# Performance work log

Hardware: AMD Instinct MI355X
Metric: run time of the kernel (lower is better)

Reference implementation:

```python
import jax, jax.numpy as jnp
import numpy as np

TEMPERATURE = 0.07
EPS = 1e-8  # torch CosineSimilarity eps


def setup_inputs() -> dict:
    key = jax.random.key(0)
    k1, k2, k3 = jax.random.split(key, 3)
    N, D = 8192, 512
    features = jax.random.normal(k1, (N, D), dtype=jnp.float32)
    positive_mask = jax.random.randint(k2, (N, N), 0, 2, dtype=jnp.int32)
    negative_mask = jax.random.randint(k3, (N, N), 0, 2, dtype=jnp.int32)
    return {"features": features, "positive_mask": positive_mask, "negative_mask": negative_mask}


def reference(features, positive_mask, negative_mask):
    N = positive_mask.shape[0]
    self_contrast = 1.0 - jnp.eye(N, dtype=features.dtype)  # zero diagonal
    pos = positive_mask.astype(features.dtype) * self_contrast  # [N, N]
    neg = negative_mask.astype(features.dtype) * self_contrast  # [N, N]

    # cosine similarity via normalized matmul (same math as broadcasted CosineSimilarity)
    norm = jnp.maximum(jnp.linalg.norm(features, axis=1, keepdims=True), EPS)
    fn = features / norm  # [N, D]
    sim = jnp.matmul(fn, fn.T) / TEMPERATURE  # [N, N]

    logits_max = jax.lax.stop_gradient(jnp.max(sim, axis=1, keepdims=True))
    e = jnp.exp(sim - logits_max)  # [N, N]

    positives = e * pos
    log_neg_sum = jnp.log(jnp.sum(e * neg, axis=1, keepdims=True))  # [N, 1]
    log_prob = positives - log_neg_sum  # [N, N] (faithful to source: exp-masked, not log)

    cardinal = jnp.sum(pos, axis=1)
    cardinal = jnp.where(cardinal == 0, 1.0, cardinal)
    log_prob_sum = jnp.sum(log_prob * pos, axis=1)
    loss = -log_prob_sum / cardinal
    return jnp.mean(loss)
```

## Files before the change

kernel.cpp:

```cpp
#include <hip/hip_runtime.h>
#include <hip/hip_bf16.h>
#include <math.h>

#define NN 8192
#define DD 512
#define INV_T 14.285714285714286f

typedef __attribute__((ext_vector_type(8))) short s16x8;
typedef __attribute__((ext_vector_type(4))) float f32x4;
typedef __attribute__((ext_vector_type(4))) int   i32x4;

__device__ __forceinline__ unsigned short f32_to_bf16(float f) {
  unsigned int u = __float_as_uint(f);
  u += 0x7FFFu + ((u >> 16) & 1u);
  return (unsigned short)(u >> 16);
}

__device__ __forceinline__ void async16(const void* g, void* l) {
  __builtin_amdgcn_global_load_lds((__attribute__((address_space(1))) void*)(void*)g,
                                   (__attribute__((address_space(3))) void*)l,
                                   16, 0, 0);
}

__global__ __launch_bounds__(256) void normalize_kernel(const float* __restrict__ f,
                                                        unsigned short* __restrict__ fnb) {
  const int wave = threadIdx.x >> 6;
  const int lane = threadIdx.x & 63;
  const int row  = blockIdx.x * 4 + wave;
  const float* src = f + (size_t)row * DD + lane * 8;
  float4 v0 = *(const float4*)src;
  float4 v1 = *(const float4*)(src + 4);
  float ss = v0.x*v0.x + v0.y*v0.y + v0.z*v0.z + v0.w*v0.w
           + v1.x*v1.x + v1.y*v1.y + v1.z*v1.z + v1.w*v1.w;
  #pragma unroll
  for (int o = 32; o; o >>= 1) ss += __shfl_xor(ss, o);
  const float r = 1.0f / fmaxf(sqrtf(ss), 1e-8f);
  ushort4 a, b;
  a.x = f32_to_bf16(v0.x * r); a.y = f32_to_bf16(v0.y * r);
  a.z = f32_to_bf16(v0.z * r); a.w = f32_to_bf16(v0.w * r);
  b.x = f32_to_bf16(v1.x * r); b.y = f32_to_bf16(v1.y * r);
  b.z = f32_to_bf16(v1.z * r); b.w = f32_to_bf16(v1.w * r);
  unsigned short* dst = fnb + (size_t)row * DD + lane * 8;
  *(ushort4*)dst = a;
  *(ushort4*)(dst + 4) = b;
}

__global__ __launch_bounds__(256, 3) void fused_kernel(const unsigned short* __restrict__ fnb,
                                                       const int* __restrict__ posm,
                                                       const int* __restrict__ negm,
                                                       float* __restrict__ Spos,
                                                       float* __restrict__ Sneg,
                                                       float* __restrict__ Pcnt) {
  const int bid = blockIdx.x;
  int bi = (int)(64.5 - sqrt(64.5 * 64.5 - 2.0 * (double)bid));
  while (64 * bi - bi * (bi - 1) / 2 > bid) --bi;
  while (64 * (bi + 1) - (bi + 1) * bi / 2 <= bid) ++bi;
  const int bj = bi + (bid - (64 * bi - bi * (bi - 1) / 2));
  const int I = bi * 128;
  const int J = bj * 128;
  const bool offdiag = (bi != bj);

  const int tid  = threadIdx.x;
  const int wave = tid >> 6;
  const int lane = tid & 63;
  const int wm = wave >> 1;
  const int wn = wave & 1;
  const int q   = lane >> 4;
  const int c16 = lane & 15;

  __shared__ alignas(16) unsigned short lA[128 * 32];
  __shared__ alignas(16) unsigned short lB[128 * 32];
  __shared__ float sacc[2][128][3];
  for (int t = tid; t < 2 * 128 * 3; t += 256) ((float*)sacc)[t] = 0.f;

  f32x4 acc[4][4];
  const f32x4 z4 = {0.f, 0.f, 0.f, 0.f};
  #pragma unroll
  for (int mt = 0; mt < 4; ++mt)
    #pragma unroll
    for (int nt = 0; nt < 4; ++nt) acc[mt][nt] = z4;

  for (int kk = 0; kk < DD / 32; ++kk) {
    const int k0 = kk * 32;
    #pragma unroll
    for (int c = 0; c < 2; ++c) {
      const int fidx = tid + c * 256;
      const int L    = fidx >> 2;
      const int p    = fidx & 3;
      const int csrc = (p ^ ((L >> 1) & 3)) & 3;
      async16(fnb + (size_t)(I + L) * DD + k0 + csrc * 8, (char*)lA + fidx * 16);
      const int gB = 4 * (L & 31) + (L >> 5);
      async16(fnb + (size_t)(J + gB) * DD + k0 + csrc * 8, (char*)lB + fidx * 16);
    }
    __syncthreads();

    s16x8 aF[4], bF[4];
    #pragma unroll
    for (int t = 0; t < 4; ++t) {
      const int arow = wm * 64 + t * 16 + c16;
      const int apos = (q ^ ((arow >> 1) & 3)) & 3;
      aF[t] = *(const s16x8*)((const char*)lA + arow * 64 + apos * 16);
      const int Lb = (wn * 16 + c16) | (t << 5);
      const int bpos = (q ^ ((Lb >> 1) & 3)) & 3;
      bF[t] = *(const s16x8*)((const char*)lB + Lb * 64 + bpos * 16);
    }
    #pragma unroll
    for (int mt = 0; mt < 4; ++mt)
      #pragma unroll
      for (int nt = 0; nt < 4; ++nt)
        acc[mt][nt] = __builtin_amdgcn_mfma_f32_16x16x32_bf16(aF[mt], bF[nt], acc[mt][nt], 0, 0, 0);
    __syncthreads();
  }

  #pragma unroll
  for (int mt = 0; mt < 4; ++mt)
    #pragma unroll
    for (int nt = 0; nt < 4; ++nt)
      #pragma unroll
      for (int r = 0; r < 4; ++r)
        acc[mt][nt][r] = __expf(acc[mt][nt][r] * INV_T - INV_T);

  const bool hasdiag = (bi == bj) && (wm == wn);
  const int cb = wn * 64 + 4 * c16;

  #pragma unroll
  for (int mt = 0; mt < 4; ++mt) {
    const int rl = wm * 64 + mt * 16 + q * 4;
    i32x4 pv[4], nv[4];
    #pragma unroll
    for (int r = 0; r < 4; ++r) {
      const size_t off = (size_t)(I + rl + r) * NN + J + cb;
      pv[r] = __builtin_nontemporal_load((const i32x4*)(posm + off));
      nv[r] = __builtin_nontemporal_load((const i32x4*)(negm + off));
    }
    #pragma unroll
    for (int r = 0; r < 4; ++r) {
      float dsp = 0.f, dsn = 0.f, dpc = 0.f;
      #pragma unroll
      for (int nt = 0; nt < 4; ++nt) {
        float pf = (float)pv[r][nt];
        float nf = (float)nv[r][nt];
        if (hasdiag && (rl + r == cb + nt)) { pf = 0.f; nf = 0.f; }
        const float e = acc[mt][nt][r];
        dsp = fmaf(e, pf, dsp);
        dsn = fmaf(e, nf, dsn);
        dpc += pf;
      }
      #pragma unroll
      for (int o = 1; o <= 8; o <<= 1) {
        dsp += __shfl_xor(dsp, o);
        dsn += __shfl_xor(dsn, o);
        dpc += __shfl_xor(dpc, o);
      }
      if (c16 == 0) {
        atomicAdd(&sacc[0][rl + r][0], dsp);
        atomicAdd(&sacc[0][rl + r][1], dsn);
        atomicAdd(&sacc[0][rl + r][2], dpc);
      }
    }
  }

  if (offdiag) {
    #pragma unroll
    for (int nt = 0; nt < 4; ++nt) {
      const int trl = cb + nt;
      i32x4 pv[4], nv[4];
      #pragma unroll
      for (int mt = 0; mt < 4; ++mt) {
        const size_t off = (size_t)(J + trl) * NN + I + wm * 64 + mt * 16 + q * 4;
        pv[mt] = __builtin_nontemporal_load((const i32x4*)(posm + off));
        nv[mt] = __builtin_nontemporal_load((const i32x4*)(negm + off));
      }
      float ts = 0.f, tn = 0.f, tp = 0.f;
      #pragma unroll
      for (int mt = 0; mt < 4; ++mt) {
        #pragma unroll
        for (int r = 0; r < 4; ++r) {
          const float e = acc[mt][nt][r];
          ts = fmaf(e, (float)pv[mt][r], ts);
          tn = fmaf(e, (float)nv[mt][r], tn);
          tp += (float)pv[mt][r];
        }
      }
      ts += __shfl_xor(ts, 16); ts += __shfl_xor(ts, 32);
      tn += __shfl_xor(tn, 16); tn += __shfl_xor(tn, 32);
      tp += __shfl_xor(tp, 16); tp += __shfl_xor(tp, 32);
      if (q == 0) {
        atomicAdd(&sacc[1][trl][0], ts);
        atomicAdd(&sacc[1][trl][1], tn);
        atomicAdd(&sacc[1][trl][2], tp);
      }
    }
  }

  __syncthreads();

  const int r = tid & 127;
  if (tid < 128) {
    atomicAdd(&Spos[I + r], sacc[0][r][0]);
    atomicAdd(&Sneg[I + r], sacc[0][r][1]);
    atomicAdd(&Pcnt[I + r], sacc[0][r][2]);
  } else if (offdiag) {
    atomicAdd(&Spos[J + r], sacc[1][r][0]);
    atomicAdd(&Sneg[J + r], sacc[1][r][1]);
    atomicAdd(&Pcnt[J + r], sacc[1][r][2]);
  }
}

__global__ __launch_bounds__(256) void finalize_kernel(const float* __restrict__ Spos,
                                                       const float* __restrict__ Sneg,
                                                       const float* __restrict__ Pcnt,
                                                       float* __restrict__ out) {
  float local = 0.f;
  for (int i = threadIdx.x; i < NN; i += 256) {
    const float sp = Spos[i], sn = Sneg[i], pc = Pcnt[i];
    const float card = (pc == 0.f) ? 1.f : pc;
    local += (logf(sn) * pc - sp) / card;
  }
  #pragma unroll
  for (int o = 32; o; o >>= 1) local += __shfl_xor(local, o);
  __shared__ float red[4];
  if ((threadIdx.x & 63) == 0) red[threadIdx.x >> 6] = local;
  __syncthreads();
  if (threadIdx.x == 0)
    out[0] = (red[0] + red[1] + red[2] + red[3]) * (1.0f / (float)NN);
}

extern "C" void kernel_launch(void* const* d_in, const int* in_sizes, int n_in,
                              void* d_out, int out_size, void* d_ws, size_t ws_size,
                              hipStream_t stream) {
  const float* feat = (const float*)d_in[0];
  const int* posm   = (const int*)d_in[1];
  const int* negm   = (const int*)d_in[2];
  float* out = (float*)d_out;

  char* ws = (char*)d_ws;
  unsigned short* fnb = (unsigned short*)ws;
  float* Spos = (float*)(ws + (size_t)8 * 1024 * 1024);
  float* Sneg = Spos + NN;
  float* Pcnt = Sneg + NN;

  hipMemsetAsync(Spos, 0, 3 * NN * sizeof(float), stream);
  normalize_kernel<<<NN / 4, 256, 0, stream>>>(feat, fnb);
  fused_kernel<<<2080, 256, 0, stream>>>(fnb, posm, negm, Spos, Sneg, Pcnt);
  finalize_kernel<<<1, 256, 0, stream>>>(Spos, Sneg, Pcnt, out);
}
```

Before: 548.6 us.

## Split GEMM into two row halves and overlap mask loads with second half

Splits the 128x128 tile GEMM into two 64-row halves, each with a K step of 64 and an 8-way XOR-swizzled LDS layout. After the first half finishes, its exp values are computed and the direct and transposed mask loads for those rows are issued and consumed while the second half's GEMM runs. The intent is to hide the large int32 mask memory traffic behind MFMA work. In exchange, B tiles are reloaded twice, the launch-bounds occupancy hint drops from 3 to 2, and more registers stay live at once.

```diff
diff --git a/kernel.cpp b/kernel.cpp
--- a/kernel.cpp
+++ b/kernel.cpp
@@ -45,7 +45,7 @@
   *(ushort4*)(dst + 4) = b;
 }
 
-__global__ __launch_bounds__(256, 3) void fused_kernel(const unsigned short* __restrict__ fnb,
+__global__ __launch_bounds__(256, 2) void fused_kernel(const unsigned short* __restrict__ fnb,
                                                        const int* __restrict__ posm,
                                                        const int* __restrict__ negm,
                                                        float* __restrict__ Spos,
@@ -68,8 +68,8 @@
   const int q   = lane >> 4;
   const int c16 = lane & 15;
 
-  __shared__ alignas(16) unsigned short lA[128 * 32];
-  __shared__ alignas(16) unsigned short lB[128 * 32];
+  __shared__ alignas(16) unsigned short lA[64 * 64];
+  __shared__ alignas(16) unsigned short lB[128 * 64];
   __shared__ float sacc[2][128][3];
   for (int t = tid; t < 2 * 128 * 3; t += 256) ((float*)sacc)[t] = 0.f;
 
@@ -80,68 +80,33 @@
     #pragma unroll
     for (int nt = 0; nt < 4; ++nt) acc[mt][nt] = z4;
 
-  for (int kk = 0; kk < DD / 32; ++kk) {
-    const int k0 = kk * 32;
-    #pragma unroll
-    for (int c = 0; c < 2; ++c) {
-      const int fidx = tid + c * 256;
-      const int L    = fidx >> 2;
-      const int p    = fidx & 3;
-      const int csrc = (p ^ ((L >> 1) & 3)) & 3;
-      async16(fnb + (size_t)(I + L) * DD + k0 + csrc * 8, (char*)lA + fidx * 16);
-      const int gB = 4 * (L & 31) + (L >> 5);
-      async16(fnb + (size_t)(J + gB) * DD + k0 + csrc * 8, (char*)lB + fidx * 16);
-    }
-    __syncthreads();
-
-    s16x8 aF[4], bF[4];
-    #pragma unroll
-    for (int t = 0; t < 4; ++t) {
-      const int arow = wm * 64 + t * 16 + c16;
-      const int apos = (q ^ ((arow >> 1) & 3)) & 3;
-      aF[t] = *(const s16x8*)((const char*)lA + arow * 64 + apos * 16);
-      const int Lb = (wn * 16 + c16) | (t << 5);
-      const int bpos = (q ^ ((Lb >> 1) & 3)) & 3;
-      bF[t] = *(const s16x8*)((const char*)lB + Lb * 64 + bpos * 16);
-    }
-    #pragma unroll
-    for (int mt = 0; mt < 4; ++mt)
-      #pragma unroll
-      for (int nt = 0; nt < 4; ++nt)
-        acc[mt][nt] = __builtin_amdgcn_mfma_f32_16x16x32_bf16(aF[mt], bF[nt], acc[mt][nt], 0, 0, 0);
-    __syncthreads();
-  }
-
-  #pragma unroll
-  for (int mt = 0; mt < 4; ++mt)
-    #pragma unroll
-    for (int nt = 0; nt < 4; ++nt)
-      #pragma unroll
-      for (int r = 0; r < 4; ++r)
-        acc[mt][nt][r] = __expf(acc[mt][nt][r] * INV_T - INV_T);
-
   const bool hasdiag = (bi == bj) && (wm == wn);
   const int cb = wn * 64 + 4 * c16;
 
-  #pragma unroll
-  for (int mt = 0; mt < 4; ++mt) {
-    const int rl = wm * 64 + mt * 16 + q * 4;
-    i32x4 pv[4], nv[4];
+  i32x4 dP[2][4], dN[2][4];
+  i32x4 tP[4][2], tN[4][2];
+  float ts[4] = {0,0,0,0}, tn[4] = {0,0,0,0}, tp[4] = {0,0,0,0};
+
+  auto dIssue = [&](int m) {
+    const int rl = wm * 64 + m * 16 + q * 4;
     #pragma unroll
     for (int r = 0; r < 4; ++r) {
       const size_t off = (size_t)(I + rl + r) * NN + J + cb;
-      pv[r] = __builtin_nontemporal_load((const i32x4*)(posm + off));
-      nv[r] = __builtin_nontemporal_load((const i32x4*)(negm + off));
-    }
+      dP[m & 1][r] = __builtin_nontemporal_load((const i32x4*)(posm + off));
+      dN[m & 1][r] = __builtin_nontemporal_load((const i32x4*)(negm + off));
+    }
+  };
+  auto dDrain = [&](int m) {
+    const int rl = wm * 64 + m * 16 + q * 4;
     #pragma unroll
     for (int r = 0; r < 4; ++r) {
       float dsp = 0.f, dsn = 0.f, dpc = 0.f;
       #pragma unroll
       for (int nt = 0; nt < 4; ++nt) {
-        float pf = (float)pv[r][nt];
-        float nf = (float)nv[r][nt];
+        float pf = (float)dP[m & 1][r][nt];
+        float nf = (float)dN[m & 1][r][nt];
         if (hasdiag && (rl + r == cb + nt)) { pf = 0.f; nf = 0.f; }
-        const float e = acc[mt][nt][r];
+        const float e = acc[m][nt][r];
         dsp = fmaf(e, pf, dsp);
         dsn = fmaf(e, nf, dsn);
         dpc += pf;
@@ -158,37 +123,128 @@
         atomicAdd(&sacc[0][rl + r][2], dpc);
       }
     }
-  }
-
+  };
+  auto tIssue = [&](int nt, int mh) {
+    #pragma unroll
+    for (int m2 = 0; m2 < 2; ++m2) {
+      const size_t off = (size_t)(J + cb + nt) * NN + I + wm * 64 + (mh * 2 + m2) * 16 + q * 4;
+      tP[nt][m2] = __builtin_nontemporal_load((const i32x4*)(posm + off));
+      tN[nt][m2] = __builtin_nontemporal_load((const i32x4*)(negm + off));
+    }
+  };
+  auto tDrain = [&](int nt, int mh) {
+    #pragma unroll
+    for (int m2 = 0; m2 < 2; ++m2) {
+      const int m = mh * 2 + m2;
+      #pragma unroll
+      for (int r = 0; r < 4; ++r) {
+        const float e  = acc[m][nt][r];
+        const float pf = (float)tP[nt][m2][r];
+        ts[nt] = fmaf(e, pf, ts[nt]);
+        tn[nt] = fmaf(e, (float)tN[nt][m2][r], tn[nt]);
+        tp[nt] += pf;
+      }
+    }
+  };
+
+  auto stage = [&](int h, int kk) {
+    const int k0 = kk * 64;
+    #pragma unroll
+    for (int c = 0; c < 2; ++c) {
+      const int fidx = tid + c * 256;
+      const int L = fidx >> 3, p = fidx & 7;
+      const int cs = p ^ (L & 7);
+      async16(fnb + (size_t)(I + (L >> 5) * 64 + h * 32 + (L & 31)) * DD + k0 + cs * 8,
+              (char*)lA + fidx * 16);
+    }
+    #pragma unroll
+    for (int c = 0; c < 4; ++c) {
+      const int fidx = tid + c * 256;
+      const int L = fidx >> 3, p = fidx & 7;
+      const int cs = p ^ (L & 7);
+      async16(fnb + (size_t)(J + 4 * (L & 31) + (L >> 5)) * DD + k0 + cs * 8,
+              (char*)lB + fidx * 16);
+    }
+  };
+  auto gemmstep = [&](int h) {
+    #pragma unroll
+    for (int ks = 0; ks < 2; ++ks) {
+      s16x8 aF[2], bF[4];
+      #pragma unroll
+      for (int mt2 = 0; mt2 < 2; ++mt2) {
+        const int La = wm * 32 + mt2 * 16 + c16;
+        const int cc = (ks * 4 + q) ^ (La & 7);
+        aF[mt2] = *(const s16x8*)((const char*)lA + La * 128 + cc * 16);
+      }
+      #pragma unroll
+      for (int t = 0; t < 4; ++t) {
+        const int Lb = wn * 16 + c16 + 32 * t;
+        const int cc = (ks * 4 + q) ^ (Lb & 7);
+        bF[t] = *(const s16x8*)((const char*)lB + Lb * 128 + cc * 16);
+      }
+      #pragma unroll
+      for (int mt2 = 0; mt2 < 2; ++mt2)
+        #pragma unroll
+        for (int nt = 0; nt < 4; ++nt)
+          acc[h * 2 + mt2][nt] =
+              __builtin_amdgcn_mfma_f32_16x16x32_bf16(aF[mt2], bF[nt], acc[h * 2 + mt2][nt], 0, 0, 0);
+    }
+  };
+
+  for (int kk = 0; kk < 8; ++kk) {
+    stage(0, kk);
+    __syncthreads();
+    gemmstep(0);
+    __syncthreads();
+  }
+  #pragma unroll
+  for (int mt = 0; mt < 2; ++mt)
+    #pragma unroll
+    for (int nt = 0; nt < 4; ++nt)
+      #pragma unroll
+      for (int r = 0; r < 4; ++r)
+        acc[mt][nt][r] = __expf(acc[mt][nt][r] * INV_T - INV_T);
+
+  #pragma unroll
+  for (int kk = 0; kk < 8; ++kk) {
+    stage(1, kk);
+    if (kk == 0) dIssue(0);
+    if (kk == 1) dIssue(1);
+    if (kk == 2 && offdiag) { tIssue(0, 0); tIssue(1, 0); }
+    if (kk == 3 && offdiag) { tIssue(2, 0); tIssue(3, 0); }
+    __syncthreads();
+    gemmstep(1);
+    if (kk == 1) dDrain(0);
+    if (kk == 2) dDrain(1);
+    if (kk == 3 && offdiag) { tDrain(0, 0); tDrain(1, 0); }
+    if (kk == 4 && offdiag) { tDrain(2, 0); tDrain(3, 0); }
+    __syncthreads();
+  }
+  #pragma unroll
+  for (int mt = 2; mt < 4; ++mt)
+    #pragma unroll
+    for (int nt = 0; nt < 4; ++nt)
+      #pragma unroll
+      for (int r = 0; r < 4; ++r)
+        acc[mt][nt][r] = __expf(acc[mt][nt][r] * INV_T - INV_T);
+
+  dIssue(2); dIssue(3);
+  dDrain(2); dDrain(3);
   if (offdiag) {
+    tIssue(0, 1); tIssue(1, 1);
+    tDrain(0, 1); tDrain(1, 1);
+    tIssue(2, 1); tIssue(3, 1);
+    tDrain(2, 1); tDrain(3, 1);
     #pragma unroll
     for (int nt = 0; nt < 4; ++nt) {
-      const int trl = cb + nt;
-      i32x4 pv[4], nv[4];
-      #pragma unroll
-      for (int mt = 0; mt < 4; ++mt) {
-        const size_t off = (size_t)(J + trl) * NN + I + wm * 64 + mt * 16 + q * 4;
-        pv[mt] = __builtin_nontemporal_load((const i32x4*)(posm + off));
-        nv[mt] = __builtin_nontemporal_load((const i32x4*)(negm + off));
-      }
-      float ts = 0.f, tn = 0.f, tp = 0.f;
-      #pragma unroll
-      for (int mt = 0; mt < 4; ++mt) {
-        #pragma unroll
-        for (int r = 0; r < 4; ++r) {
-          const float e = acc[mt][nt][r];
-          ts = fmaf(e, (float)pv[mt][r], ts);
-          tn = fmaf(e, (float)nv[mt][r], tn);
-          tp += (float)pv[mt][r];
-        }
-      }
-      ts += __shfl_xor(ts, 16); ts += __shfl_xor(ts, 32);
-      tn += __shfl_xor(tn, 16); tn += __shfl_xor(tn, 32);
-      tp += __shfl_xor(tp, 16); tp += __shfl_xor(tp, 32);
+      float a = ts[nt], b = tn[nt], p = tp[nt];
+      a += __shfl_xor(a, 16); a += __shfl_xor(a, 32);
+      b += __shfl_xor(b, 16); b += __shfl_xor(b, 32);
+      p += __shfl_xor(p, 16); p += __shfl_xor(p, 32);
       if (q == 0) {
-        atomicAdd(&sacc[1][trl][0], ts);
-        atomicAdd(&sacc[1][trl][1], tn);
-        atomicAdd(&sacc[1][trl][2], tp);
+        atomicAdd(&sacc[1][cb + nt][0], a);
+        atomicAdd(&sacc[1][cb + nt][1], b);
+        atomicAdd(&sacc[1][cb + nt][2], p);
       }
     }
   }
```

Measured after the change: 571.5 us. 4.2% more time.

## Warp-specialize fused kernel: mask-loader waves build bitmaps while MFMA waves compute

Applied to the files above, without the earlier changes.

Doubles the block to 512 threads. Four waves run the bf16 MFMA similarity tile while four others stream the positive and negative mask tiles, direct and transposed. The loader waves compress the masks into 64-bit ballot bitmaps in LDS, and the epilogue reads bits and uses popcount for the positive counts. The aim is to overlap the dominant mask-read traffic with the GEMM instead of loading masks only after it finishes. The risks are lower occupancy from the larger block, matching barrier counts between the two wave roles, and intricate bit-index mapping that must agree with the changed B-tile row layout.

```diff
diff --git a/kernel.cpp b/kernel.cpp
--- a/kernel.cpp
+++ b/kernel.cpp
@@ -45,7 +45,7 @@
   *(ushort4*)(dst + 4) = b;
 }
 
-__global__ __launch_bounds__(256, 3) void fused_kernel(const unsigned short* __restrict__ fnb,
+__global__ __launch_bounds__(512, 4) void fused_kernel(const unsigned short* __restrict__ fnb,
                                                        const int* __restrict__ posm,
                                                        const int* __restrict__ negm,
                                                        float* __restrict__ Spos,
@@ -63,132 +63,173 @@
   const int tid  = threadIdx.x;
   const int wave = tid >> 6;
   const int lane = tid & 63;
-  const int wm = wave >> 1;
-  const int wn = wave & 1;
-  const int q   = lane >> 4;
-  const int c16 = lane & 15;
 
   __shared__ alignas(16) unsigned short lA[128 * 32];
   __shared__ alignas(16) unsigned short lB[128 * 32];
+  __shared__ unsigned long long bdir[2][128][2];
+  __shared__ unsigned long long btr [2][128][2];
   __shared__ float sacc[2][128][3];
-  for (int t = tid; t < 2 * 128 * 3; t += 256) ((float*)sacc)[t] = 0.f;
+  for (int t = tid; t < 2 * 128 * 3; t += 512) ((float*)sacc)[t] = 0.f;
 
   f32x4 acc[4][4];
-  const f32x4 z4 = {0.f, 0.f, 0.f, 0.f};
-  #pragma unroll
-  for (int mt = 0; mt < 4; ++mt)
-    #pragma unroll
-    for (int nt = 0; nt < 4; ++nt) acc[mt][nt] = z4;
-
-  for (int kk = 0; kk < DD / 32; ++kk) {
-    const int k0 = kk * 32;
-    #pragma unroll
-    for (int c = 0; c < 2; ++c) {
-      const int fidx = tid + c * 256;
-      const int L    = fidx >> 2;
-      const int p    = fidx & 3;
-      const int csrc = (p ^ ((L >> 1) & 3)) & 3;
-      async16(fnb + (size_t)(I + L) * DD + k0 + csrc * 8, (char*)lA + fidx * 16);
-      const int gB = 4 * (L & 31) + (L >> 5);
-      async16(fnb + (size_t)(J + gB) * DD + k0 + csrc * 8, (char*)lB + fidx * 16);
-    }
-    __syncthreads();
-
-    s16x8 aF[4], bF[4];
-    #pragma unroll
-    for (int t = 0; t < 4; ++t) {
-      const int arow = wm * 64 + t * 16 + c16;
-      const int apos = (q ^ ((arow >> 1) & 3)) & 3;
-      aF[t] = *(const s16x8*)((const char*)lA + arow * 64 + apos * 16);
-      const int Lb = (wn * 16 + c16) | (t << 5);
-      const int bpos = (q ^ ((Lb >> 1) & 3)) & 3;
-      bF[t] = *(const s16x8*)((const char*)lB + Lb * 64 + bpos * 16);
-    }
+
+  if (wave < 4) {
+    const int wm = wave >> 1, wn = wave & 1;
+    const int q = lane >> 4, c16 = lane & 15;
+    const f32x4 z4 = {0.f, 0.f, 0.f, 0.f};
     #pragma unroll
     for (int mt = 0; mt < 4; ++mt)
       #pragma unroll
+      for (int nt = 0; nt < 4; ++nt) acc[mt][nt] = z4;
+
+    for (int kk = 0; kk < DD / 32; ++kk) {
+      const int k0 = kk * 32;
+      #pragma unroll
+      for (int c = 0; c < 2; ++c) {
+        const int fidx = tid + c * 256;
+        const int row  = fidx >> 2;
+        const int p    = fidx & 3;
+        const int csrc = (p ^ ((row >> 1) & 3)) & 3;
+        async16(fnb + (size_t)(I + row) * DD + k0 + csrc * 8, (char*)lA + fidx * 16);
+        async16(fnb + (size_t)(J + row) * DD + k0 + csrc * 8, (char*)lB + fidx * 16);
+      }
+      __syncthreads();
+
+      s16x8 aF[4], bF[4];
+      #pragma unroll
+      for (int t = 0; t < 4; ++t) {
+        const int arow = wm * 64 + t * 16 + c16;
+        const int apos = (q ^ ((arow >> 1) & 3)) & 3;
+        aF[t] = *(const s16x8*)((const char*)lA + arow * 64 + apos * 16);
+        const int brow = wn * 64 + t * 16 + c16;
+        const int bpos = (q ^ ((brow >> 1) & 3)) & 3;
+        bF[t] = *(const s16x8*)((const char*)lB + brow * 64 + bpos * 16);
+      }
+      #pragma unroll
+      for (int mt = 0; mt < 4; ++mt)
+        #pragma unroll
+        for (int nt = 0; nt < 4; ++nt)
+          acc[mt][nt] = __builtin_amdgcn_mfma_f32_16x16x32_bf16(aF[mt], bF[nt], acc[mt][nt], 0, 0, 0);
+      __syncthreads();
+    }
+    #pragma unroll
+    for (int mt = 0; mt < 4; ++mt)
+      #pragma unroll
       for (int nt = 0; nt < 4; ++nt)
-        acc[mt][nt] = __builtin_amdgcn_mfma_f32_16x16x32_bf16(aF[mt], bF[nt], acc[mt][nt], 0, 0, 0);
-    __syncthreads();
-  }
-
-  #pragma unroll
-  for (int mt = 0; mt < 4; ++mt)
-    #pragma unroll
-    for (int nt = 0; nt < 4; ++nt)
-      #pragma unroll
-      for (int r = 0; r < 4; ++r)
-        acc[mt][nt][r] = __expf(acc[mt][nt][r] * INV_T - INV_T);
-
-  const bool hasdiag = (bi == bj) && (wm == wn);
-  const int cb = wn * 64 + 4 * c16;
-
-  #pragma unroll
-  for (int mt = 0; mt < 4; ++mt) {
-    const int rl = wm * 64 + mt * 16 + q * 4;
-    i32x4 pv[4], nv[4];
-    #pragma unroll
-    for (int r = 0; r < 4; ++r) {
-      const size_t off = (size_t)(I + rl + r) * NN + J + cb;
-      pv[r] = __builtin_nontemporal_load((const i32x4*)(posm + off));
-      nv[r] = __builtin_nontemporal_load((const i32x4*)(negm + off));
-    }
-    #pragma unroll
-    for (int r = 0; r < 4; ++r) {
-      float dsp = 0.f, dsn = 0.f, dpc = 0.f;
+        #pragma unroll
+        for (int r = 0; r < 4; ++r)
+          acc[mt][nt][r] = __expf(acc[mt][nt][r] * INV_T - INV_T);
+  } else {
+    const int mw   = wave - 4;
+    const int msel = mw & 1;
+    const int half = mw >> 1;
+    const int* mb  = msel ? negm : posm;
+    const int sub  = lane >> 5;
+    const int col4 = (lane & 31) * 4;
+
+    i32x4 vbuf[2][2];
+
+    #define MLOAD(g)                                                          \
+      if ((g) < 32 && !((g) >= 16 && !offdiag)) {                             \
+        const int R0 = ((g) < 16) ? I : J;                                    \
+        const int C0 = ((g) < 16) ? J : I;                                    \
+        _Pragma("unroll")                                                     \
+        for (int u = 0; u < 2; ++u) {                                         \
+          const int rl = half * 64 + ((g) & 15) * 4 + 2 * u + sub;            \
+          vbuf[(g) & 1][u] = __builtin_nontemporal_load(                      \
+              (const i32x4*)(mb + (size_t)(R0 + rl) * NN + C0 + col4));       \
+        }                                                                     \
+      }
+
+    MLOAD(0)
+    #pragma unroll
+    for (int g = 0; g < 32; ++g) {
+      MLOAD(g + 1)
+      __syncthreads();
+      if (!(g >= 16 && !offdiag)) {
+        unsigned long long (*dst)[2] = (g < 16) ? bdir[msel] : btr[msel];
+        #pragma unroll
+        for (int u = 0; u < 2; ++u) {
+          const i32x4 v = vbuf[g & 1][u];
+          const unsigned long long b0 = __ballot(v.x != 0);
+          const unsigned long long b1 = __ballot(v.y != 0);
+          const unsigned long long b2 = __ballot(v.z != 0);
+          const unsigned long long b3 = __ballot(v.w != 0);
+          if (lane < 4) {
+            const int s = lane >> 1, h = lane & 1;
+            const int k = 16 * (2 * s + h);
+            const unsigned long long t =
+                ((b0 >> k) & 0xFFFFull)         | (((b1 >> k) & 0xFFFFull) << 16)
+              | (((b2 >> k) & 0xFFFFull) << 32) | (((b3 >> k) & 0xFFFFull) << 48);
+            dst[half * 64 + (g & 15) * 4 + 2 * u + s][h] = t;
+          }
+        }
+      }
+    }
+  }
+
+  __syncthreads();
+
+  if (wave < 4) {
+    const int wm = wave >> 1, wn = wave & 1;
+    const int q = lane >> 4, c16 = lane & 15;
+    const bool hasdiag = (bi == bj) && (wm == wn);
+
+    const int shd = (c16 >> 2) + (c16 & 3) * 16;
+    #pragma unroll
+    for (int mt = 0; mt < 4; ++mt) {
+      const int rl = wm * 64 + mt * 16 + q * 4;
+      #pragma unroll
+      for (int r = 0; r < 4; ++r) {
+        unsigned long long wp = bdir[0][rl + r][wn];
+        unsigned long long wnn = bdir[1][rl + r][wn];
+        if (hasdiag) {
+          const unsigned long long m = ~(1ULL << (mt * 4 + q + 16 * r));
+          wp &= m; wnn &= m;
+        }
+        float dsp = 0.f, dsn = 0.f;
+        #pragma unroll
+        for (int nt = 0; nt < 4; ++nt) {
+          const float e = acc[mt][nt][r];
+          dsp = fmaf(e, (float)((wp  >> (nt * 4 + shd)) & 1ULL), dsp);
+          dsn = fmaf(e, (float)((wnn >> (nt * 4 + shd)) & 1ULL), dsn);
+        }
+        #pragma unroll
+        for (int o = 1; o <= 8; o <<= 1) {
+          dsp += __shfl_xor(dsp, o);
+          dsn += __shfl_xor(dsn, o);
+        }
+        if (c16 == 0) {
+          atomicAdd(&sacc[0][rl + r][0], dsp);
+          atomicAdd(&sacc[0][rl + r][1], dsn);
+          atomicAdd(&sacc[0][rl + r][2], (float)__popcll(wp));
+        }
+      }
+    }
+    if (offdiag) {
       #pragma unroll
       for (int nt = 0; nt < 4; ++nt) {
-        float pf = (float)pv[r][nt];
-        float nf = (float)nv[r][nt];
-        if (hasdiag && (rl + r == cb + nt)) { pf = 0.f; nf = 0.f; }
-        const float e = acc[mt][nt][r];
-        dsp = fmaf(e, pf, dsp);
-        dsn = fmaf(e, nf, dsn);
-        dpc += pf;
-      }
-      #pragma unroll
-      for (int o = 1; o <= 8; o <<= 1) {
-        dsp += __shfl_xor(dsp, o);
-        dsn += __shfl_xor(dsn, o);
-        dpc += __shfl_xor(dpc, o);
-      }
-      if (c16 == 0) {
-        atomicAdd(&sacc[0][rl + r][0], dsp);
-        atomicAdd(&sacc[0][rl + r][1], dsn);
-        atomicAdd(&sacc[0][rl + r][2], dpc);
-      }
-    }
-  }
-
-  if (offdiag) {
-    #pragma unroll
-    for (int nt = 0; nt < 4; ++nt) {
-      const int trl = cb + nt;
-      i32x4 pv[4], nv[4];
-      #pragma unroll
-      for (int mt = 0; mt < 4; ++mt) {
-        const size_t off = (size_t)(J + trl) * NN + I + wm * 64 + mt * 16 + q * 4;
-        pv[mt] = __builtin_nontemporal_load((const i32x4*)(posm + off));
-        nv[mt] = __builtin_nontemporal_load((const i32x4*)(negm + off));
-      }
-      float ts = 0.f, tn = 0.f, tp = 0.f;
-      #pragma unroll
-      for (int mt = 0; mt < 4; ++mt) {
-        #pragma unroll
-        for (int r = 0; r < 4; ++r) {
-          const float e = acc[mt][nt][r];
-          ts = fmaf(e, (float)pv[mt][r], ts);
-          tn = fmaf(e, (float)nv[mt][r], tn);
-          tp += (float)pv[mt][r];
-        }
-      }
-      ts += __shfl_xor(ts, 16); ts += __shfl_xor(ts, 32);
-      tn += __shfl_xor(tn, 16); tn += __shfl_xor(tn, 32);
-      tp += __shfl_xor(tp, 16); tp += __shfl_xor(tp, 32);
-      if (q == 0) {
-        atomicAdd(&sacc[1][trl][0], ts);
-        atomicAdd(&sacc[1][trl][1], tn);
-        atomicAdd(&sacc[1][trl][2], tp);
+        const int cl = wn * 64 + nt * 16 + c16;
+        const unsigned long long tpw = btr[0][cl][wm];
+        const unsigned long long tnw = btr[1][cl][wm];
+        float ts = 0.f, tn = 0.f;
+        #pragma unroll
+        for (int mt = 0; mt < 4; ++mt) {
+          const int sh = mt * 4 + q;
+          #pragma unroll
+          for (int r = 0; r < 4; ++r) {
+            const float e = acc[mt][nt][r];
+            ts = fmaf(e, (float)((tpw >> (sh + 16 * r)) & 1ULL), ts);
+            tn = fmaf(e, (float)((tnw >> (sh + 16 * r)) & 1ULL), tn);
+          }
+        }
+        ts += __shfl_xor(ts, 16); ts += __shfl_xor(ts, 32);
+        tn += __shfl_xor(tn, 16); tn += __shfl_xor(tn, 32);
+        if (q == 0) {
+          atomicAdd(&sacc[1][cl][0], ts);
+          atomicAdd(&sacc[1][cl][1], tn);
+          atomicAdd(&sacc[1][cl][2], (float)__popcll(tpw));
+        }
       }
     }
   }
@@ -200,7 +241,7 @@
     atomicAdd(&Spos[I + r], sacc[0][r][0]);
     atomicAdd(&Sneg[I + r], sacc[0][r][1]);
     atomicAdd(&Pcnt[I + r], sacc[0][r][2]);
-  } else if (offdiag) {
+  } else if (tid < 256 && offdiag) {
     atomicAdd(&Spos[J + r], sacc[1][r][0]);
     atomicAdd(&Sneg[J + r], sacc[1][r][1]);
     atomicAdd(&Pcnt[J + r], sacc[1][r][2]);
@@ -242,6 +283,6 @@
 
   hipMemsetAsync(Spos, 0, 3 * NN * sizeof(float), stream);
   normalize_kernel<<<NN / 4, 256, 0, stream>>>(feat, fnb);
-  fused_kernel<<<2080, 256, 0, stream>>>(fnb, posm, negm, Spos, Sneg, Pcnt);
+  fused_kernel<<<2080, 512, 0, stream>>>(fnb, posm, negm, Spos, Sneg, Pcnt);
   finalize_kernel<<<1, 256, 0, stream>>>(Spos, Sneg, Pcnt, out);
 }
```

New measurement: 593.2 us. +8.1%, slower.
